# Performance work log

Measured on AMD Instinct MI355X. Metric: run time of the kernel, lower is better.

## Reference

```python
import jax, jax.numpy as jnp
import numpy as np

D_MODEL = 1024
N_HEADS = 16
D_K = D_MODEL // N_HEADS
THETA = 10000.0


def _rope(x, token_positions):
    # x: [b, h, s, d_k]; interleaved RoPE (pairs at even/odd positions)
    half = D_K // 2
    inv_freq = 1.0 / (THETA ** (2.0 * jnp.arange(half, dtype=jnp.float32) / D_K))  # [half]
    angles = token_positions.astype(jnp.float32)[:, None] * inv_freq[None, :]      # [s, half]
    sin, cos = jnp.sin(angles), jnp.cos(angles)
    x_even = x[..., 0::2]
    x_odd = x[..., 1::2]
    out_even = cos * x_even - sin * x_odd
    out_odd = sin * x_even + cos * x_odd
    # interleave back: [..., half, 2] -> [..., d_k]
    return jnp.stack((out_even, out_odd), axis=-1).reshape(x.shape)


def setup_inputs() -> dict:
    key = jax.random.key(0)
    kx, kq, kk, kv, ko = jax.random.split(key, 5)
    b, s = 4, 2048
    std = (2.0 / (D_MODEL + D_MODEL)) ** 0.5
    return {
        "x": jax.random.normal(kx, (b, s, D_MODEL), dtype=jnp.float32),
        "Wq": jax.random.normal(kq, (D_MODEL, D_MODEL), dtype=jnp.float32) * std,
        "Wk": jax.random.normal(kk, (D_MODEL, D_MODEL), dtype=jnp.float32) * std,
        "Wv": jax.random.normal(kv, (D_MODEL, D_MODEL), dtype=jnp.float32) * std,
        "Wo": jax.random.normal(ko, (D_MODEL, D_MODEL), dtype=jnp.float32) * std,
        "token_positions": jnp.arange(s, dtype=jnp.int32),
    }


def reference(x, Wq, Wk, Wv, Wo, token_positions):
    b, s, _ = x.shape
    split = lambda t: t.reshape(b, s, N_HEADS, D_K).transpose(0, 2, 1, 3)  # b h s d
    q = split(x @ Wq.T)
    k = split(x @ Wk.T)
    v = split(x @ Wv.T)
    q = _rope(q, token_positions)
    k = _rope(k, token_positions)
    scores = jnp.einsum("bhnd,bhmd->bhnm", q, k) / jnp.sqrt(jnp.float32(D_K))
    causal = jnp.tril(jnp.ones((s, s), dtype=bool))
    scores = jnp.where(causal, scores, -jnp.inf)
    attn = jax.nn.softmax(scores, axis=-1)
    out = jnp.einsum("bhnm,bhmd->bhnd", attn, v)
    out = out.transpose(0, 2, 1, 3).reshape(b, s, D_MODEL)
    return out @ Wo.T
```

## Files before the change

### kernel.cpp

```cpp
#include <hip/hip_runtime.h>
#include <stdint.h>

typedef __attribute__((ext_vector_type(8))) __bf16 bf16x8;
typedef __attribute__((ext_vector_type(4))) float f32x4;
typedef __attribute__((ext_vector_type(16))) float f32x16;
typedef __attribute__((ext_vector_type(8))) unsigned short ushort8;

__device__ __forceinline__ unsigned short f2bf(float f){
  union { float f; unsigned int i; } v; v.f = f;
  unsigned int r = v.i + 0x7fffu + ((v.i >> 16) & 1u);
  return (unsigned short)(r >> 16);
}
__device__ __forceinline__ void gload16(const void* g, void* l){
  __builtin_amdgcn_global_load_lds((__attribute__((address_space(1))) void*)(g),
                                   (__attribute__((address_space(3))) void*)(l),
                                   16, 0, 0);
}
__device__ __forceinline__ unsigned int cvtpk(float lo, float hi){
  unsigned int r;
  asm("v_cvt_pk_bf16_f32 %0, %1, %2" : "=v"(r) : "v"(lo), "v"(hi));
  return r;
}
__device__ __forceinline__ bf16x8 ldsw(const char* tile, int row, int colb){
  return *(const bf16x8*)(tile + row*128 + (colb ^ ((row & 7) << 4)));
}

#define SEQ   2048
#define DM    1024
#define NH    16
#define DK    64
#define BATCH 4
#define MTOT  (BATCH*SEQ)
#define NX    (MTOT*DM)
#define NW    (DM*DM)

#define QSCALE 0.18033688011112f

__global__ __launch_bounds__(256) void k_tables(const int* __restrict__ pos,
                                                float* __restrict__ tab)
{
  const int idx = blockIdx.x * 256 + threadIdx.x;
  const int s = idx >> 5, i = idx & 31;
  const float inv = __expf(-0.28782313662425575f * (float)i);
  const float a = (float)pos[s] * inv;
  tab[2*idx]   = cosf(a);
  tab[2*idx+1] = sinf(a);
}

__global__ __launch_bounds__(256) void k_convert(
    const float* __restrict__ x,  const float* __restrict__ wq,
    const float* __restrict__ wk, const float* __restrict__ wv,
    const float* __restrict__ wo,
    unsigned short* __restrict__ xb, unsigned short* __restrict__ wb)
{
  const long long tid = (long long)blockIdx.x * 256 + threadIdx.x;
  const long long e = tid * 4;
  const float* src; unsigned short* dst;
  if (e < NX) { src = x + e; dst = xb + e; }
  else {
    long long j = e - NX;
    int seg = (int)(j >> 20);
    long long off = j & 1048575;
    src = (seg==0?wq:seg==1?wk:seg==2?wv:wo) + off;
    dst = wb + (size_t)seg*NW + off;
  }
  float4 v = *(const float4*)src;
  unsigned long long pk =  (unsigned long long)f2bf(v.x)
                        | ((unsigned long long)f2bf(v.y) << 16)
                        | ((unsigned long long)f2bf(v.z) << 32)
                        | ((unsigned long long)f2bf(v.w) << 48);
  *(unsigned long long*)dst = pk;
}

#define BK 32
#define NTK (DM/BK)

template<int MODE>
__global__ __launch_bounds__(512, 3) void k_gemm(
    const unsigned short* __restrict__ A,
    const unsigned short* __restrict__ Wb,
    unsigned short* __restrict__ D0,
    unsigned short* __restrict__ D1,
    unsigned short* __restrict__ D2,
    float* __restrict__ Dout,
    const float* __restrict__ tab)
{
  __shared__ __attribute__((aligned(16))) unsigned short As[2][256*BK];
  __shared__ __attribute__((aligned(16))) unsigned short Bs[2][128*BK];
  const int tid  = threadIdx.x;
  const int lane = tid & 63;
  const int w    = tid >> 6;
  const int wm = w >> 1, wn = w & 1;
  const int m0 = blockIdx.x * 256;
  const int n0 = blockIdx.y * 128;

  const int z = (MODE == 0) ? blockIdx.z : 0;
  const unsigned short* W = Wb + (size_t)z * NW;
  unsigned short* Dh = (MODE == 0) ? ((z == 0) ? D0 : (z == 1) ? D1 : D2) : nullptr;
  const bool vtr = (MODE == 0) && (z == 2);

  f32x4 acc[4][4];
  #pragma unroll
  for (int i = 0; i < 4; ++i)
    #pragma unroll
    for (int j = 0; j < 4; ++j)
      acc[i][j] = (f32x4)0.0f;

  auto stage = [&](int buf, int t){
    const int k0 = t * BK;
    #pragma unroll
    for (int cc = 0; cc < 2; ++cc){
      const int f = cc*512 + tid;
      const int row = f >> 2, kc = f & 3;
      const int kcs = kc ^ ((row >> 1) & 3);
      gload16(A + (size_t)(m0 + row)*DM + k0 + kcs*8,
              (char*)&As[buf][0] + (cc*512 + w*64)*16);
    }
    {
      const int row = tid >> 2, kc = tid & 3;
      const int kcs = kc ^ ((row >> 1) & 3);
      gload16(W + (size_t)(n0 + row)*DM + k0 + kcs*8,
              (char*)&Bs[buf][0] + (w*64)*16);
    }
  };

  stage(0, 0);
  __syncthreads();
  int cur = 0;
  for (int t = 0; t < NTK; ++t){
    if (t + 1 < NTK) stage(cur ^ 1, t + 1);
    const char* Ab_ = (const char*)&As[cur][0];
    const char* Bb_ = (const char*)&Bs[cur][0];
    bf16x8 af[4], bfr[4];
    #pragma unroll
    for (int i = 0; i < 4; ++i){
      const int rowA = wm*64 + i*16 + (lane & 15);
      const int rowB = wn*64 + i*16 + (lane & 15);
      af[i]  = *(const bf16x8*)(Ab_ + rowA*64 + ((((lane >> 4) ^ (rowA >> 1)) & 3) << 4));
      bfr[i] = *(const bf16x8*)(Bb_ + rowB*64 + ((((lane >> 4) ^ (rowB >> 1)) & 3) << 4));
    }
    #pragma unroll
    for (int i = 0; i < 4; ++i)
      #pragma unroll
      for (int j = 0; j < 4; ++j)
        acc[i][j] = __builtin_amdgcn_mfma_f32_16x16x32_bf16(af[i], bfr[j], acc[i][j], 0, 0, 0);
    __syncthreads();
    cur ^= 1;
  }

  if (MODE == 0 && !vtr){
    const float scale = (z == 0) ? QSCALE : 1.0f;
    #pragma unroll
    for (int i = 0; i < 4; ++i)
      #pragma unroll
      for (int j = 0; j < 4; ++j)
        #pragma unroll
        for (int r = 0; r < 4; ++r){
          const int m = m0 + wm*64 + i*16 + ((lane >> 4) << 2) + r;
          const int n = n0 + wn*64 + j*16 + (lane & 15);
          const float v  = acc[i][j][r];
          const float vp = __shfl_xor(v, 1, 64);
          const int sp = m & 2047, d = n & 63;
          const float2 cs = ((const float2*)tab)[sp*32 + (d >> 1)];
          const float o = ((n & 1) ? (cs.y*vp + cs.x*v) : (cs.x*v - cs.y*vp)) * scale;
          const int b = m >> 11, hh = n >> 6;
          *(__bf16*)&Dh[((size_t)((b*NH + hh)*SEQ + sp))*DK + d] = (__bf16)o;
        }
  } else {
    #pragma unroll
    for (int i = 0; i < 4; ++i)
      #pragma unroll
      for (int j = 0; j < 4; ++j)
        #pragma unroll
        for (int r = 0; r < 4; ++r){
          const int m = m0 + wm*64 + i*16 + ((lane >> 4) << 2) + r;
          const int n = n0 + wn*64 + j*16 + (lane & 15);
          if (MODE == 0){
            const int b = m >> 11, sp = m & 2047, hh = n >> 6, d = n & 63;
            *(__bf16*)&Dh[(((size_t)(b*NH + hh))*DK + d)*SEQ + sp] = (__bf16)acc[i][j][r];
          } else {
            Dout[(size_t)m * DM + n] = acc[i][j][r];
          }
        }
  }
}

__global__ __launch_bounds__(512, 4) void k_attn(const unsigned short* __restrict__ Qh,
                                                 const unsigned short* __restrict__ Kh,
                                                 const unsigned short* __restrict__ Vt,
                                                 unsigned short* __restrict__ Ab)
{
  __shared__ uint4 ldsu[4096];
  char* base = (char*)ldsu;
  const int tid  = threadIdx.x;
  const int lane = tid & 63;
  const int w    = tid >> 6;
  const int ww   = w & 3;
  const int g    = w >> 2;
  const int tl   = tid & 255;
  const int l31  = lane & 31;
  const int hl   = lane >> 5;
  char* gb = base + g*32768;

  const int jj = blockIdx.x, bh = blockIdx.y;
  const unsigned short* Qb = Qh + (size_t)bh*(SEQ*DK);
  const unsigned short* Kb = Kh + (size_t)bh*(SEQ*DK);
  const unsigned short* Vb = Vt + (size_t)bh*(SEQ*DK);
  const int b = bh >> 4, hd = bh & 15;

  for (int pass = 0; pass < 2; ++pass){
    const int qt = pass ? jj : 15 - jj;
    const int q0 = qt * 128;
    const int qbase = q0 + ww*32;

    bf16x8 qf[4];
    #pragma unroll
    for (int t = 0; t < 4; ++t)
      qf[t] = *(const bf16x8*)(Qb + (size_t)(qbase + l31)*DK + t*16 + hl*8);

    f32x16 acc0 = (f32x16)0.0f, acc1 = (f32x16)0.0f;
    float lsum = 0.0f;

    const int nk = qt + 1;
    const int tbase = g * nk;
    const int wqmax = qbase + 31;

    auto stage = [&](int buf, int ktile){
      const int k0s = ktile * 64;
      char* Kd = gb + buf*16384;
      char* Vd = Kd + 8192;
      #pragma unroll
      for (int cc = 0; cc < 2; ++cc){
        const int f = cc*256 + tl;
        const int r = f >> 3, slot = f & 7;
        const int sw = ((slot ^ (r & 7)) << 3);
        gload16(Kb + (size_t)(k0s + r)*DK + sw, Kd + (cc*256 + ww*64)*16);
        gload16(Vb + (size_t)r*SEQ + k0s + sw, Vd + (cc*256 + ww*64)*16);
      }
    };

    if (pass) __syncthreads();
    stage(0, tbase);
    __syncthreads();
    int cur = 0;

    for (int kt = 0; kt < nk; ++kt){
      const int k0 = (tbase + kt) * 64;
      if (kt + 1 < nk) stage(cur ^ 1, tbase + kt + 1);
      if (k0 <= wqmax){
        const char* Ks = gb + cur*16384;
        const char* Vs = Ks + 8192;

        f32x16 sv0 = (f32x16)0.0f, sv1 = (f32x16)0.0f;
        #pragma unroll
        for (int t = 0; t < 4; ++t){
          const int colb = t*32 + hl*16;
          const bf16x8 a0 = ldsw(Ks, l31, colb);
          const bf16x8 a1 = ldsw(Ks, 32 + l31, colb);
          sv0 = __builtin_amdgcn_mfma_f32_32x32x16_bf16(a0, qf[t], sv0, 0, 0, 0);
          sv1 = __builtin_amdgcn_mfma_f32_32x32x16_bf16(a1, qf[t], sv1, 0, 0, 0);
        }

        if (k0 + 63 > qbase){
          const int q = qbase + l31;
          #pragma unroll
          for (int j = 0; j < 16; ++j){
            const int kv = k0 + (j&3) + 8*(j>>2) + 4*hl;
            if (kv > q)      sv0[j] = -1e30f;
            if (kv + 32 > q) sv1[j] = -1e30f;
          }
        }

        #pragma unroll
        for (int j = 0; j < 16; ++j){
          sv0[j] = exp2f(sv0[j]);
          sv1[j] = exp2f(sv1[j]);
        }
        float ts[8];
        #pragma unroll
        for (int j = 0; j < 8; ++j)
          ts[j] = (sv0[j] + sv0[j+8]) + (sv1[j] + sv1[j+8]);
        #pragma unroll
        for (int off = 4; off; off >>= 1)
          #pragma unroll
          for (int j = 0; j < off; ++j)
            ts[j] += ts[j+off];
        lsum += ts[0] + __shfl_xor(ts[0], 32, 64);

        #pragma unroll
        for (int t = 0; t < 4; ++t){
          f32x16& s = (t < 2) ? sv0 : sv1;
          const int b0v = (t & 1) * 8;
          const unsigned int A0 = cvtpk(s[b0v+0], s[b0v+1]);
          const unsigned int A1 = cvtpk(s[b0v+2], s[b0v+3]);
          const unsigned int B0 = cvtpk(s[b0v+4], s[b0v+5]);
          const unsigned int B1 = cvtpk(s[b0v+6], s[b0v+7]);
          const unsigned int s0 = hl ? A0 : B0;
          const unsigned int s1 = hl ? A1 : B1;
          const unsigned int r0 = (unsigned int)__shfl_xor((int)s0, 32, 64);
          const unsigned int r1 = (unsigned int)__shfl_xor((int)s1, 32, 64);
          union { unsigned int u[4]; bf16x8 v; } f;
          f.u[0] = hl ? r0 : A0; f.u[1] = hl ? r1 : A1;
          f.u[2] = hl ? B0 : r0; f.u[3] = hl ? B1 : r1;
          const int colb = t*32 + hl*16;
          const bf16x8 v0 = ldsw(Vs, l31, colb);
          const bf16x8 v1 = ldsw(Vs, 32 + l31, colb);
          acc0 = __builtin_amdgcn_mfma_f32_32x32x16_bf16(v0, f.v, acc0, 0, 0, 0);
          acc1 = __builtin_amdgcn_mfma_f32_32x32x16_bf16(v1, f.v, acc1, 0, 0, 0);
        }
      }
      __syncthreads();
      cur ^= 1;
    }

    if (g == 1){
      char* cw = base + ww*9216 + lane*144;
      #pragma unroll
      for (int q4 = 0; q4 < 4; ++q4){
        *(f32x4*)(cw + q4*16)      = (f32x4){acc0[4*q4], acc0[4*q4+1], acc0[4*q4+2], acc0[4*q4+3]};
        *(f32x4*)(cw + 64 + q4*16) = (f32x4){acc1[4*q4], acc1[4*q4+1], acc1[4*q4+2], acc1[4*q4+3]};
      }
      *(float*)(cw + 128) = lsum;
    }
    __syncthreads();
    if (g == 0){
      const char* cr = base + ww*9216 + lane*144;
      const float l1 = *(const float*)(cr + 128);
      const float linv = 1.0f / (lsum + l1);
      unsigned short* orow = Ab + ((size_t)(b*SEQ + qbase + l31))*DM + hd*DK;
      #pragma unroll
      for (int mt = 0; mt < 2; ++mt){
        #pragma unroll
        for (int g4 = 0; g4 < 4; ++g4){
          const f32x16& a = mt ? acc1 : acc0;
          const f32x4 o = *(const f32x4*)(cr + mt*64 + g4*16);
          const unsigned int u0 = cvtpk((a[4*g4+0] + o[0])*linv, (a[4*g4+1] + o[1])*linv);
          const unsigned int u1 = cvtpk((a[4*g4+2] + o[2])*linv, (a[4*g4+3] + o[3])*linv);
          *(unsigned long long*)(orow + mt*32 + g4*8 + hl*4) =
              (unsigned long long)u0 | ((unsigned long long)u1 << 32);
        }
      }
    }
  }
}

extern "C" void kernel_launch(void* const* d_in, const int* in_sizes, int n_in,
                              void* d_out, int out_size, void* d_ws, size_t ws_size,
                              hipStream_t stream)
{
  (void)in_sizes; (void)n_in; (void)out_size;
  const float* x  = (const float*)d_in[0];
  const float* wq = (const float*)d_in[1];
  const float* wk = (const float*)d_in[2];
  const float* wv = (const float*)d_in[3];
  const float* wo = (const float*)d_in[4];
  const int* pos  = (const int*)d_in[5];
  float* out = (float*)d_out;

  if (ws_size < 92800000u) return;
  char* ws = (char*)d_ws;
  unsigned short* xb = (unsigned short*)(ws);
  unsigned short* wb = (unsigned short*)(ws + 16777216);
  unsigned short* Qh = (unsigned short*)(ws + 25165824);
  unsigned short* Kh = (unsigned short*)(ws + 41943040);
  unsigned short* Vt = (unsigned short*)(ws + 75497472);
  float* tab         = (float*)(ws + 92274688);

  k_tables  <<<256, 256, 0, stream>>>(pos, tab);
  k_convert <<<12288, 256, 0, stream>>>(x, wq, wk, wv, wo, xb, wb);
  k_gemm<0> <<<dim3(32, 8, 3), 512, 0, stream>>>(xb, wb, Qh, Kh, Vt, nullptr, tab);
  k_attn    <<<dim3(8, 64), 512, 0, stream>>>(Qh, Kh, Vt, xb);
  k_gemm<1> <<<dim3(32, 8, 1), 512, 0, stream>>>(xb, wb + 3*NW, nullptr, nullptr,
                                                 nullptr, out, nullptr);
}
```

Measured before the change: 188.5 us.

## Remap GEMM blocks for XCD locality, widen convert, add MFMA priority hints

Replaces the 3D GEMM grid with a flattened 1D grid whose index remapping places neighbouring M tiles on the same XCD (bid&7 chosen as the major M index), so blocks that share B tiles can reuse L2. The convert kernel now handles 8 floats per thread with 16-byte stores and launches half as many blocks. The attention kernel raises wave priority around its MFMA sections with s_setprio so matrix work is issued ahead of other waves. Each of these is a separate scheduling tweak; the remap assumes the round-robin dispatch of blocks across XCDs.

```diff
diff --git a/kernel.cpp b/kernel.cpp
--- a/kernel.cpp
+++ b/kernel.cpp
@@ -53,8 +53,8 @@
     const float* __restrict__ wo,
     unsigned short* __restrict__ xb, unsigned short* __restrict__ wb)
 {
-  const long long tid = (long long)blockIdx.x * 256 + threadIdx.x;
-  const long long e = tid * 4;
+  const int tid = blockIdx.x * 256 + threadIdx.x;
+  const long long e = (long long)tid * 8;
   const float* src; unsigned short* dst;
   if (e < NX) { src = x + e; dst = xb + e; }
   else {
@@ -64,12 +64,14 @@
     src = (seg==0?wq:seg==1?wk:seg==2?wv:wo) + off;
     dst = wb + (size_t)seg*NW + off;
   }
-  float4 v = *(const float4*)src;
-  unsigned long long pk =  (unsigned long long)f2bf(v.x)
-                        | ((unsigned long long)f2bf(v.y) << 16)
-                        | ((unsigned long long)f2bf(v.z) << 32)
-                        | ((unsigned long long)f2bf(v.w) << 48);
-  *(unsigned long long*)dst = pk;
+  const float4 a = *(const float4*)src;
+  const float4 b = *(const float4*)(src + 4);
+  uint4 o;
+  o.x = (unsigned int)f2bf(a.x) | ((unsigned int)f2bf(a.y) << 16);
+  o.y = (unsigned int)f2bf(a.z) | ((unsigned int)f2bf(a.w) << 16);
+  o.z = (unsigned int)f2bf(b.x) | ((unsigned int)f2bf(b.y) << 16);
+  o.w = (unsigned int)f2bf(b.z) | ((unsigned int)f2bf(b.w) << 16);
+  *(uint4*)dst = o;
 }
 
 #define BK 32
@@ -91,10 +93,14 @@
   const int lane = tid & 63;
   const int w    = tid >> 6;
   const int wm = w >> 1, wn = w & 1;
-  const int m0 = blockIdx.x * 256;
-  const int n0 = blockIdx.y * 128;
-
-  const int z = (MODE == 0) ? blockIdx.z : 0;
+
+  const int bid = blockIdx.x;
+  const int tq  = bid >> 3;
+  const int m0  = ((bid & 7)*4 + (tq & 3)) * 256;
+  const int r   = tq >> 2;
+  const int n0  = (MODE == 0 ? (r & 7) : r) * 128;
+  const int z   = (MODE == 0) ? (r >> 3) : 0;
+
   const unsigned short* W = Wb + (size_t)z * NW;
   unsigned short* Dh = (MODE == 0) ? ((z == 0) ? D0 : (z == 1) ? D1 : D2) : nullptr;
   const bool vtr = (MODE == 0) && (z == 2);
@@ -155,10 +161,10 @@
       #pragma unroll
       for (int j = 0; j < 4; ++j)
         #pragma unroll
-        for (int r = 0; r < 4; ++r){
-          const int m = m0 + wm*64 + i*16 + ((lane >> 4) << 2) + r;
+        for (int rr = 0; rr < 4; ++rr){
+          const int m = m0 + wm*64 + i*16 + ((lane >> 4) << 2) + rr;
           const int n = n0 + wn*64 + j*16 + (lane & 15);
-          const float v  = acc[i][j][r];
+          const float v  = acc[i][j][rr];
           const float vp = __shfl_xor(v, 1, 64);
           const int sp = m & 2047, d = n & 63;
           const float2 cs = ((const float2*)tab)[sp*32 + (d >> 1)];
@@ -172,14 +178,14 @@
       #pragma unroll
       for (int j = 0; j < 4; ++j)
         #pragma unroll
-        for (int r = 0; r < 4; ++r){
-          const int m = m0 + wm*64 + i*16 + ((lane >> 4) << 2) + r;
+        for (int rr = 0; rr < 4; ++rr){
+          const int m = m0 + wm*64 + i*16 + ((lane >> 4) << 2) + rr;
           const int n = n0 + wn*64 + j*16 + (lane & 15);
           if (MODE == 0){
             const int b = m >> 11, sp = m & 2047, hh = n >> 6, d = n & 63;
-            *(__bf16*)&Dh[(((size_t)(b*NH + hh))*DK + d)*SEQ + sp] = (__bf16)acc[i][j][r];
+            *(__bf16*)&Dh[(((size_t)(b*NH + hh))*DK + d)*SEQ + sp] = (__bf16)acc[i][j][rr];
           } else {
-            Dout[(size_t)m * DM + n] = acc[i][j][r];
+            Dout[(size_t)m * DM + n] = acc[i][j][rr];
           }
         }
   }
@@ -252,6 +258,7 @@
         const char* Vs = Ks + 8192;
 
         f32x16 sv0 = (f32x16)0.0f, sv1 = (f32x16)0.0f;
+        __builtin_amdgcn_s_setprio(1);
         #pragma unroll
         for (int t = 0; t < 4; ++t){
           const int colb = t*32 + hl*16;
@@ -260,6 +267,7 @@
           sv0 = __builtin_amdgcn_mfma_f32_32x32x16_bf16(a0, qf[t], sv0, 0, 0, 0);
           sv1 = __builtin_amdgcn_mfma_f32_32x32x16_bf16(a1, qf[t], sv1, 0, 0, 0);
         }
+        __builtin_amdgcn_s_setprio(0);
 
         if (k0 + 63 > qbase){
           const int q = qbase + l31;
@@ -287,6 +295,7 @@
             ts[j] += ts[j+off];
         lsum += ts[0] + __shfl_xor(ts[0], 32, 64);
 
+        __builtin_amdgcn_s_setprio(1);
         #pragma unroll
         for (int t = 0; t < 4; ++t){
           f32x16& s = (t < 2) ? sv0 : sv1;
@@ -308,6 +317,7 @@
           acc0 = __builtin_amdgcn_mfma_f32_32x32x16_bf16(v0, f.v, acc0, 0, 0, 0);
           acc1 = __builtin_amdgcn_mfma_f32_32x32x16_bf16(v1, f.v, acc1, 0, 0, 0);
         }
+        __builtin_amdgcn_s_setprio(0);
       }
       __syncthreads();
       cur ^= 1;
@@ -367,9 +377,9 @@
   float* tab         = (float*)(ws + 92274688);
 
   k_tables  <<<256, 256, 0, stream>>>(pos, tab);
-  k_convert <<<12288, 256, 0, stream>>>(x, wq, wk, wv, wo, xb, wb);
-  k_gemm<0> <<<dim3(32, 8, 3), 512, 0, stream>>>(xb, wb, Qh, Kh, Vt, nullptr, tab);
+  k_convert <<<6144, 256, 0, stream>>>(x, wq, wk, wv, wo, xb, wb);
+  k_gemm<0> <<<768, 512, 0, stream>>>(xb, wb, Qh, Kh, Vt, nullptr, tab);
   k_attn    <<<dim3(8, 64), 512, 0, stream>>>(Qh, Kh, Vt, xb);
-  k_gemm<1> <<<dim3(32, 8, 1), 512, 0, stream>>>(xb, wb + 3*NW, nullptr, nullptr,
-                                                 nullptr, out, nullptr);
-}
+  k_gemm<1> <<<256, 512, 0, stream>>>(xb, wb + 3*NW, nullptr, nullptr,
+                                      nullptr, out, nullptr);
+}
```

New measurement: 189.5 us. No clear change (+0.5%).
